# Performance work log

Measured on AMD Instinct MI355X. Metric: run time of the kernel, lower is better.

The kernel has to match this reference:

```python
import jax, jax.numpy as jnp
import numpy as np

N = 10000      # nodes (attention_adj_matrix_shape = (N, N))
E = 320000     # edges, avg degree 32
D_IN = 256     # input feature dim
D_H = 256      # hidden_units = [256]
ALPHA = 0.2    # leaky_relu slope for attention activation


def setup_inputs() -> dict:
    key = jax.random.key(0)
    k_x, k_src, k_dst, k_w1, k_b1, k_wa, k_ba = jax.random.split(key, 7)
    node_features = jax.random.normal(k_x, (N, D_IN), dtype=jnp.float32)
    # edges sorted by source column (tf.math.segment_sum requires sorted segment ids)
    src = jnp.sort(jax.random.randint(k_src, (E,), 0, N))
    dst = jax.random.randint(k_dst, (E,), 0, N)
    edges = jnp.stack([src, dst], axis=1).astype(jnp.int64)
    # hidden_layer: single Dense(256) (linear, keras Dense default activation=None)
    W1 = jax.random.normal(k_w1, (D_IN, D_H), dtype=jnp.float32) / np.sqrt(D_IN)
    b1 = jnp.zeros((D_H,), dtype=jnp.float32)
    # attention_layer: Dense(1) then activation
    Wa = jax.random.normal(k_wa, (2 * D_H, 1), dtype=jnp.float32) / np.sqrt(2 * D_H)
    ba = jnp.zeros((1,), dtype=jnp.float32)
    return {"node_features": node_features, "edges": edges,
            "W1": W1, "b1": b1, "Wa": Wa, "ba": ba}


def reference(node_features, edges, W1, b1, Wa, ba):
    n = node_features.shape[0]
    # hidden projection
    feats = node_features @ W1 + b1                       # [N, D_H]
    src, dst = edges[:, 0], edges[:, 1]
    # pairwise gather + concat: [E, 2*D_H]
    pair = jnp.concatenate([feats[src], feats[dst]], axis=1)
    scores = jax.nn.leaky_relu((pair @ Wa + ba)[:, 0], ALPHA)  # [E]
    # segment softmax over source node (matches exp / segment_sum / gather)
    ex = jnp.exp(scores)
    denom = jax.ops.segment_sum(ex, src, num_segments=n)       # [N]
    alpha = ex / denom[src]                                     # [E]
    # dense scatter of attention weights (scatter_nd sums duplicates)
    A = jnp.zeros((n, n), dtype=feats.dtype).at[src, dst].add(alpha)
    # add_self_features=False -> plain aggregate
    return A @ feats                                            # [N, D_H]
```

## Files before the change

kernel.cpp:

```cpp
#include <hip/hip_runtime.h>
#include <hip/hip_bf16.h>

#define N_NODES 10000
#define E_EDGES 320000
#define D 256
#define LRELU_ALPHA 0.2f


using short8  = __attribute__((ext_vector_type(8))) short;
using floatx4 = __attribute__((ext_vector_type(4))) float;
using bf16 = __hip_bfloat16;

__device__ __forceinline__ float bu2f(unsigned short u) {
    return __uint_as_float((unsigned)u << 16);
}
__device__ __forceinline__ unsigned short f2bu(float f) {
    union { bf16 b; unsigned short u; } cv;
    cv.b = __float2bfloat16(f);
    return cv.u;
}

__global__ __launch_bounds__(256) void wprep(const float* __restrict__ W1,
                                             bf16* __restrict__ W1f) {
    const int id = blockIdx.x * 256 + threadIdx.x;
    const int j = id & 7, l = (id >> 3) & 63, t = (id >> 9) & 15, s = id >> 13;
    const int k = s * 32 + (l >> 4) * 8 + j;
    const int n = t * 16 + (l & 15);
    W1f[id] = __float2bfloat16(W1[k * D + n]);
}

__global__ __launch_bounds__(256) void gemm_mfma(const float* __restrict__ X,
                                                 const bf16* __restrict__ W1f,
                                                 const float* __restrict__ b1,
                                                 const float* __restrict__ Wa,
                                                 bf16* __restrict__ featsb,
                                                 float* __restrict__ a_src,
                                                 float* __restrict__ a_dst) {
    const int w = threadIdx.x >> 6, l = threadIdx.x & 63;
    const int quad = l >> 4, lan = l & 15;
    const int row0 = blockIdx.x * 16;

    floatx4 acc[4] = {{0.f, 0.f, 0.f, 0.f}, {0.f, 0.f, 0.f, 0.f},
                      {0.f, 0.f, 0.f, 0.f}, {0.f, 0.f, 0.f, 0.f}};

    const float4* Ax = (const float4*)(X + (size_t)(row0 + lan) * D);
    const short8* B8 = (const short8*)W1f;

    #pragma unroll
    for (int s = 0; s < 8; ++s) {
        const float4 u = Ax[s * 8 + quad * 2];
        const float4 v = Ax[s * 8 + quad * 2 + 1];
        short8 af;
        af[0] = (short)f2bu(u.x); af[1] = (short)f2bu(u.y);
        af[2] = (short)f2bu(u.z); af[3] = (short)f2bu(u.w);
        af[4] = (short)f2bu(v.x); af[5] = (short)f2bu(v.y);
        af[6] = (short)f2bu(v.z); af[7] = (short)f2bu(v.w);
        #pragma unroll
        for (int t = 0; t < 4; ++t) {
            const short8 bf = B8[(s * 16 + (4 * w + t)) * 64 + l];
            acc[t] = __builtin_amdgcn_mfma_f32_16x16x32_bf16(af, bf, acc[t], 0, 0, 0);
        }
    }

    float p1[4] = {0.f, 0.f, 0.f, 0.f}, p2[4] = {0.f, 0.f, 0.f, 0.f};
    #pragma unroll
    for (int t = 0; t < 4; ++t) {
        const int n = (4 * w + t) * 16 + lan;
        const float bias = b1[n], wa1 = Wa[n], wa2 = Wa[D + n];
        #pragma unroll
        for (int r = 0; r < 4; ++r) {
            const float v = acc[t][r] + bias;
            featsb[(size_t)(row0 + quad * 4 + r) * D + n] = __float2bfloat16(v);
            p1[r] += v * wa1;
            p2[r] += v * wa2;
        }
    }

    __shared__ float red1[4][16], red2[4][16];
    #pragma unroll
    for (int r = 0; r < 4; ++r) {
        #pragma unroll
        for (int off = 1; off < 16; off <<= 1) {
            p1[r] += __shfl_xor(p1[r], off);
            p2[r] += __shfl_xor(p2[r], off);
        }
        if (lan == 0) { red1[w][quad * 4 + r] = p1[r]; red2[w][quad * 4 + r] = p2[r]; }
    }
    __syncthreads();
    if (threadIdx.x < 16) {
        const int m = threadIdx.x;
        a_src[row0 + m] = red1[0][m] + red1[1][m] + red1[2][m] + red1[3][m];
        a_dst[row0 + m] = red2[0][m] + red2[1][m] + red2[2][m] + red2[3][m];
    }
}

__global__ __launch_bounds__(256) void prep(const int* __restrict__ raw,
                                            const float* __restrict__ a_src,
                                            const float* __restrict__ a_dst,
                                            const float* __restrict__ ba,
                                            int2* __restrict__ edata,
                                            int* __restrict__ row_start) {
    bool is64 = true;
    #pragma unroll
    for (int t = 0; t < 16; ++t)
        if (raw[2 * t + 1] != 0) is64 = false;

    const int e = blockIdx.x * 256 + threadIdx.x;
    int s, d;
    if (is64) {
        const int4 v = ((const int4*)raw)[e];
        s = v.x; d = v.z;
    } else {
        const int2 v = ((const int2*)raw)[e];
        s = v.x; d = v.y;
    }
    int sprev = __shfl_up(s, 1);
    if ((threadIdx.x & 63) == 0)
        sprev = (e == 0) ? -1 : raw[is64 ? (4 * e - 4) : (2 * e - 2)];

    float sc = a_src[s] + a_dst[d] + ba[0];
    sc = (sc > 0.f) ? sc : LRELU_ALPHA * sc;
    edata[e] = make_int2(d << 9, __float_as_int(expf(sc)));

    for (int r = sprev + 1; r <= s; ++r) row_start[r] = e;
    if (e == E_EDGES - 1)
        for (int r = s + 1; r <= N_NODES; ++r) row_start[r] = E_EDGES;
}

__global__ __launch_bounds__(256) void aggregate_half(const int2* __restrict__ edata,
                                                      const int* __restrict__ row_start,
                                                      const unsigned short* __restrict__ featsb,
                                                      float* __restrict__ out,
                                                      const int half) {
    __shared__ int2 els[4][64];
    const int wv = threadIdx.x >> 6, l = threadIdx.x & 63;
    const int i = blockIdx.x * 4 + wv;
    const int rs = row_start[i], re = row_start[i + 1];
    const char* Fb = (const char*)featsb + half * 256 + l * 4;

    float2 acc = {0.f, 0.f};
    float dsum = 0.f;

    for (int e = rs; e < re; e += 64) {
        const int cnt = min(64, re - e);
        if (l < cnt) els[wv][l] = edata[e + l];
        __builtin_amdgcn_wave_barrier();

        int j = 0;
        for (; j + 8 <= cnt; j += 8) {
            #pragma unroll
            for (int u = 0; u < 8; ++u) {
                const int2 ed = els[wv][j + u];
                const unsigned int f = *(const unsigned int*)(Fb + (size_t)(unsigned)ed.x);
                const float x = __int_as_float(ed.y);
                acc.x += x * bu2f((unsigned short)(f & 0xffff));
                acc.y += x * bu2f((unsigned short)(f >> 16));
                dsum += x;
            }
        }
        for (; j < cnt; ++j) {
            const int2 ed = els[wv][j];
            const unsigned int f = *(const unsigned int*)(Fb + (size_t)(unsigned)ed.x);
            const float x = __int_as_float(ed.y);
            acc.x += x * bu2f((unsigned short)(f & 0xffff));
            acc.y += x * bu2f((unsigned short)(f >> 16));
            dsum += x;
        }
        __builtin_amdgcn_wave_barrier();
    }

    const float inv = (re > rs) ? 1.f / dsum : 0.f;
    float2 o;
    o.x = acc.x * inv;
    o.y = acc.y * inv;
    ((float2*)(out + (size_t)i * D + half * 128))[l] = o;
}

extern "C" void kernel_launch(void* const* d_in, const int* in_sizes, int n_in,
                              void* d_out, int out_size, void* d_ws, size_t ws_size,
                              hipStream_t stream) {
    const float* X     = (const float*)d_in[0];
    const int*   edges = (const int*)d_in[1];
    const float* W1    = (const float*)d_in[2];
    const float* b1    = (const float*)d_in[3];
    const float* Wa    = (const float*)d_in[4];
    const float* ba    = (const float*)d_in[5];
    float* out = (float*)d_out;

    bf16* featsb = (bf16*)d_ws;
    bf16* W1f    = featsb + (size_t)N_NODES * D;
    float* a_src = (float*)(W1f + 65536);
    float* a_dst = a_src + N_NODES;
    int2*  edata = (int2*)(a_dst + N_NODES);
    int*   row_start = (int*)(edata + E_EDGES);

    wprep<<<65536 / 256, 256, 0, stream>>>(W1, W1f);
    gemm_mfma<<<N_NODES / 16, 256, 0, stream>>>(X, W1f, b1, Wa, featsb, a_src, a_dst);
    prep<<<E_EDGES / 256, 256, 0, stream>>>(edges, a_src, a_dst, ba, edata, row_start);
    aggregate_half<<<N_NODES / 4, 256, 0, stream>>>(edata, row_start,
                                                    (const unsigned short*)featsb, out, 0);
    aggregate_half<<<N_NODES / 4, 256, 0, stream>>>(edata, row_start,
                                                    (const unsigned short*)featsb, out, 1);
}
```

Measured before the change: 106.0 us.

## Merge two half-width aggregation passes into one with 16-byte gathers

The two `aggregate_half` launches, each covering 128 feature columns with 4-byte loads, become a single `aggregate` kernel. In it, each lane gathers 16 bytes (8 bf16 values) per edge, and the two half-waves process alternating edges. Partial sums are combined with a cross-half shuffle before normalising and writing float4 outputs. This reads the edge list and row offsets once instead of twice, removes a launch, and issues wider gather loads. The cost is more accumulator registers and a padded tail loop that loads row 0 for inactive slots.

Result: no change. 104.1 us (-1.8%).

```diff
diff --git a/kernel.cpp b/kernel.cpp
--- a/kernel.cpp
+++ b/kernel.cpp
@@ -11,8 +11,8 @@
 using floatx4 = __attribute__((ext_vector_type(4))) float;
 using bf16 = __hip_bfloat16;
 
-__device__ __forceinline__ float bu2f(unsigned short u) {
-    return __uint_as_float((unsigned)u << 16);
+__device__ __forceinline__ float bu2f(unsigned int u) {
+    return __uint_as_float(u << 16);
 }
 __device__ __forceinline__ unsigned short f2bu(float f) {
     union { bf16 b; unsigned short u; } cv;
@@ -127,18 +127,19 @@
         for (int r = s + 1; r <= N_NODES; ++r) row_start[r] = E_EDGES;
 }
 
-__global__ __launch_bounds__(256) void aggregate_half(const int2* __restrict__ edata,
-                                                      const int* __restrict__ row_start,
-                                                      const unsigned short* __restrict__ featsb,
-                                                      float* __restrict__ out,
-                                                      const int half) {
+__global__ __launch_bounds__(256) void aggregate(const int2* __restrict__ edata,
+                                                 const int* __restrict__ row_start,
+                                                 const unsigned short* __restrict__ featsb,
+                                                 float* __restrict__ out) {
     __shared__ int2 els[4][64];
     const int wv = threadIdx.x >> 6, l = threadIdx.x & 63;
+    const int h = l >> 5;
+    const int c = l & 31;
     const int i = blockIdx.x * 4 + wv;
     const int rs = row_start[i], re = row_start[i + 1];
-    const char* Fb = (const char*)featsb + half * 256 + l * 4;
-
-    float2 acc = {0.f, 0.f};
+    const char* Fb = (const char*)featsb + c * 16;
+
+    float acc[8] = {0.f, 0.f, 0.f, 0.f, 0.f, 0.f, 0.f, 0.f};
     float dsum = 0.f;
 
     for (int e = rs; e < re; e += 64) {
@@ -147,33 +148,42 @@
         __builtin_amdgcn_wave_barrier();
 
         int j = 0;
-        for (; j + 8 <= cnt; j += 8) {
+        for (; j + 16 <= cnt; j += 16) {
             #pragma unroll
             for (int u = 0; u < 8; ++u) {
-                const int2 ed = els[wv][j + u];
-                const unsigned int f = *(const unsigned int*)(Fb + (size_t)(unsigned)ed.x);
+                const int2 ed = els[wv][j + 2 * u + h];
+                const uint4 f = *(const uint4*)(Fb + (size_t)(unsigned)ed.x);
                 const float x = __int_as_float(ed.y);
-                acc.x += x * bu2f((unsigned short)(f & 0xffff));
-                acc.y += x * bu2f((unsigned short)(f >> 16));
+                acc[0] += x * bu2f(f.x & 0xffff); acc[1] += x * bu2f(f.x >> 16);
+                acc[2] += x * bu2f(f.y & 0xffff); acc[3] += x * bu2f(f.y >> 16);
+                acc[4] += x * bu2f(f.z & 0xffff); acc[5] += x * bu2f(f.z >> 16);
+                acc[6] += x * bu2f(f.w & 0xffff); acc[7] += x * bu2f(f.w >> 16);
                 dsum += x;
             }
         }
-        for (; j < cnt; ++j) {
-            const int2 ed = els[wv][j];
-            const unsigned int f = *(const unsigned int*)(Fb + (size_t)(unsigned)ed.x);
+        for (; j < cnt; j += 2) {
+            const int idx = j + h;
+            const int2 ed = (idx < cnt) ? els[wv][idx] : make_int2(0, 0);
+            const uint4 f = *(const uint4*)(Fb + (size_t)(unsigned)ed.x);
             const float x = __int_as_float(ed.y);
-            acc.x += x * bu2f((unsigned short)(f & 0xffff));
-            acc.y += x * bu2f((unsigned short)(f >> 16));
+            acc[0] += x * bu2f(f.x & 0xffff); acc[1] += x * bu2f(f.x >> 16);
+            acc[2] += x * bu2f(f.y & 0xffff); acc[3] += x * bu2f(f.y >> 16);
+            acc[4] += x * bu2f(f.z & 0xffff); acc[5] += x * bu2f(f.z >> 16);
+            acc[6] += x * bu2f(f.w & 0xffff); acc[7] += x * bu2f(f.w >> 16);
             dsum += x;
         }
         __builtin_amdgcn_wave_barrier();
     }
 
+    dsum += __shfl_xor(dsum, 32);
+    #pragma unroll
+    for (int q = 0; q < 8; ++q) acc[q] += __shfl_xor(acc[q], 32);
+
     const float inv = (re > rs) ? 1.f / dsum : 0.f;
-    float2 o;
-    o.x = acc.x * inv;
-    o.y = acc.y * inv;
-    ((float2*)(out + (size_t)i * D + half * 128))[l] = o;
+    float4 o;
+    if (h == 0) { o.x = acc[0] * inv; o.y = acc[1] * inv; o.z = acc[2] * inv; o.w = acc[3] * inv; }
+    else        { o.x = acc[4] * inv; o.y = acc[5] * inv; o.z = acc[6] * inv; o.w = acc[7] * inv; }
+    *(float4*)(out + (size_t)i * D + c * 8 + h * 4) = o;
 }
 
 extern "C" void kernel_launch(void* const* d_in, const int* in_sizes, int n_in,
@@ -197,8 +207,6 @@
     wprep<<<65536 / 256, 256, 0, stream>>>(W1, W1f);
     gemm_mfma<<<N_NODES / 16, 256, 0, stream>>>(X, W1f, b1, Wa, featsb, a_src, a_dst);
     prep<<<E_EDGES / 256, 256, 0, stream>>>(edges, a_src, a_dst, ba, edata, row_start);
-    aggregate_half<<<N_NODES / 4, 256, 0, stream>>>(edata, row_start,
-                                                    (const unsigned short*)featsb, out, 0);
-    aggregate_half<<<N_NODES / 4, 256, 0, stream>>>(edata, row_start,
-                                                    (const unsigned short*)featsb, out, 1);
-}
+    aggregate<<<N_NODES / 4, 256, 0, stream>>>(edata, row_start,
+                                               (const unsigned short*)featsb, out);
+}
```
